# Kernel tuning notes

Measured on AMD Instinct MI355X. Metric: run time of the kernel, lower is better.

Reference implementation:

```python
import jax, jax.numpy as jnp
import numpy as np

LN_EPS = 1e-5


def _gather(x, idx):
    # x: [B, N, C], idx: [B, N, K] -> [B, N, K, C]
    return jax.vmap(lambda xb, ib: xb[ib])(x, idx)


def setup_inputs() -> dict:
    key = jax.random.key(0)
    ks = jax.random.split(key, 8)
    B, N, K, C_in, C_out, GEO = 2, 16384, 32, 128, 128, 10
    return {
        "points": jax.random.normal(ks[0], (B, N, 3), dtype=jnp.float32),
        "features": jax.random.normal(ks[1], (B, N, C_in), dtype=jnp.float32),
        "grouped_idx": jax.random.randint(ks[2], (B, N, K), 0, N, dtype=jnp.int32),
        "w_pos": jax.random.normal(ks[3], (GEO, C_in), dtype=jnp.float32) * (GEO ** -0.5),
        "b_pos": jnp.zeros((C_in,), jnp.float32),
        "w_gcm": jax.random.normal(ks[4], (C_in, C_in), dtype=jnp.float32) * (C_in ** -0.5),
        "b_gcm": jnp.zeros((C_in,), jnp.float32),
        "w_out": jax.random.normal(ks[5], (C_in, C_out), dtype=jnp.float32) * (C_in ** -0.5),
        "b_out": jnp.zeros((C_out,), jnp.float32),
        "ln_g": jnp.ones((C_out,), jnp.float32),
        "ln_b": jnp.zeros((C_out,), jnp.float32),
    }


def reference(points, features, grouped_idx, w_pos, b_pos, w_gcm, b_gcm,
              w_out, b_out, ln_g, ln_b):
    # gather neighbor coords and features: [B, N, K, *]
    grouped_pts = _gather(points, grouped_idx)
    xyz = points[..., 0:3]                      # [B, N, 3]
    grouped_xyz = grouped_pts[..., 0:3]         # [B, N, K, 3]
    center = xyz[:, :, None, :]                 # [B, N, 1, 3]
    diff = grouped_xyz - center                 # xi - xj
    dist = jnp.linalg.norm(diff, axis=-1, keepdims=True)  # ||xi - xj||
    K = grouped_xyz.shape[2]
    geo = jnp.concatenate(
        [jnp.broadcast_to(center, grouped_xyz.shape), grouped_xyz, diff, dist],
        axis=-1)                                # [B, N, K, 10]
    expanded_f = geo @ w_pos + b_pos            # pos_proj -> [B, N, K, C_in]
    grouped_f = _gather(features, grouped_idx)  # [B, N, K, C_in]
    h = jax.nn.relu((grouped_f + expanded_f) @ w_gcm + b_gcm)  # gcm_layer
    pooled = jnp.max(h, axis=2)                 # maxpooling over neighbors
    res = pooled + features                     # residual
    o = res @ w_out + b_out                     # out Linear
    mu = jnp.mean(o, axis=-1, keepdims=True)
    var = jnp.mean((o - mu) ** 2, axis=-1, keepdims=True)
    o = (o - mu) * jax.lax.rsqrt(var + LN_EPS) * ln_g + ln_b  # LayerNorm
    return jax.nn.relu(o)
```

## Files before the change

### kernel.cpp

```cpp
#include <hip/hip_runtime.h>
#include <hip/hip_bf16.h>
#include <math.h>

typedef __attribute__((ext_vector_type(8))) short short8;
typedef __attribute__((ext_vector_type(4))) short short4v;
typedef __attribute__((ext_vector_type(4))) float float4v;
typedef unsigned short ushort_t;

constexpr int NPTS = 32768;
constexpr int NN   = 16384;
constexpr int KK   = 32;
constexpr int CC   = 128;
constexpr int GRP  = 16;
constexpr int SG2  = 24;
constexpr int SR   = 136;
#define LN_EPS 1e-5f
#define MFMA   __builtin_amdgcn_mfma_f32_16x16x32_bf16

constexpr size_t WS_WP   = 0;
constexpr size_t WS_WO   = 40960;
constexpr size_t WS_BE   = 73728;
constexpr size_t WS_PG   = 74240;
constexpr size_t WS_FB   = 79360;
constexpr size_t WS_NEED = WS_FB + (size_t)NPTS * CC * 2;

__device__ __forceinline__ short f2bs(float x) {
    return (short)__builtin_bit_cast(unsigned short, __float2bfloat16(x));
}
__device__ __forceinline__ float bs2f(ushort_t u) {
    return __uint_as_float(((unsigned)u) << 16);
}

__global__ __launch_bounds__(128) void prep_fold(
    const float* __restrict__ w_pos, const float* __restrict__ b_pos,
    const float* __restrict__ w_gcm, const float* __restrict__ b_gcm,
    float* __restrict__ wsPG, float* __restrict__ wsBeff)
{
    const int c = threadIdx.x, g = blockIdx.x;
    if (g < 10) {
        float s = 0.f;
        #pragma unroll
        for (int r = 0; r < 128; ++r) s += w_pos[g * 128 + r] * w_gcm[r * 128 + c];
        wsPG[g * 128 + c] = s;
    } else {
        float s = b_gcm[c];
        #pragma unroll
        for (int r = 0; r < 128; ++r) s += b_pos[r] * w_gcm[r * 128 + c];
        wsBeff[c] = s;
    }
}

__global__ __launch_bounds__(256) void prep_pack(
    const float* __restrict__ features, const float* __restrict__ w_gcm,
    const float* __restrict__ w_out, const float* __restrict__ wsPG,
    short* __restrict__ wsWp, short* __restrict__ wsWo, ushort_t* __restrict__ featbf,
    int do_convert)
{
    const int t = threadIdx.x, blk = blockIdx.x;
    if (blk < 512) {
        if (!do_convert) return;
        const int base = blk * 2048 + t;
        #pragma unroll
        for (int i = 0; i < 8; ++i) {
            const int f4 = base + i * 256;
            const float4 a = ((const float4*)features)[f4];
            short4v v; v[0]=f2bs(a.x); v[1]=f2bs(a.y); v[2]=f2bs(a.z); v[3]=f2bs(a.w);
            ((short4v*)featbf)[f4] = v;
        }
        return;
    }
    if (blk == 512) {
        #pragma unroll 4
        for (int e = t; e < 16 * 128 * 8; e += 256) {
            const int j = e & 7, n = (e >> 3) & 127, g = e >> 10;
            wsWp[e] = f2bs(w_gcm[(g * 8 + j) * 128 + n]);
        }
        return;
    }
    if (blk == 513) {
        #pragma unroll 4
        for (int e2 = t; e2 < 4 * 128 * 8; e2 += 256) {
            const int e = 16 * 128 * 8 + e2;
            const int j = e & 7, n = (e >> 3) & 127, g = e >> 10;
            const int k = g * 8 + j;
            wsWp[e] = (k < 138) ? f2bs(wsPG[(k - 128) * 128 + n]) : (short)0;
        }
        return;
    }
    #pragma unroll 4
    for (int e = t; e < 128 * 128; e += 256) {
        const int j = e & 7, n = (e >> 3) & 127, g = e >> 10;
        wsWo[e] = f2bs(w_out[(g * 8 + j) * 128 + n]);
    }
}

template<int FB>
__global__ __launch_bounds__(256, 3) void bridge_main(
    const float* __restrict__ points, const float* __restrict__ features,
    const int*   __restrict__ gidx,
    const short* __restrict__ wsWp, const short* __restrict__ wsWo,
    const float* __restrict__ wsBeff, const ushort_t* __restrict__ featbf,
    const float* __restrict__ b_out, const float* __restrict__ ln_g,
    const float* __restrict__ ln_b,
    float* __restrict__ out)
{
    __shared__ short sA[4][KK * CC];
    __shared__ short sG[3][KK * SG2];
    __shared__ short sRes[GRP * SR];
    __shared__ short sResF[GRP * CC];
    __shared__ int   sIdx[GRP * KK];
    __shared__ float sCtr[GRP * 3];
    __shared__ float sPS[4][GRP], sPQ[4][GRP];

    const int t = threadIdx.x, wv = t >> 6, lane = t & 63;
    const int quad = (lane >> 4) & 3, m = lane & 15;
    const int g0 = blockIdx.x * GRP;
    const int nbase = (g0 >= NN) ? NN : 0;
    const int col0 = wv * 32 + m;

    sIdx[t]       = gidx[(size_t)g0 * KK + t];
    sIdx[t + 256] = gidx[(size_t)g0 * KK + t + 256];
    if (t < GRP * 3) sCtr[t] = points[(size_t)g0 * 3 + t];
    if constexpr (FB) {
        const ushort_t* rs = featbf + (size_t)g0 * CC + (wv * 64 + lane) * 8;
        short* rd = sResF + wv * 512;
        __builtin_amdgcn_global_load_lds((const __attribute__((address_space(1))) void*)rs,
                                         (__attribute__((address_space(3))) void*)rd, 16, 0, 0);
    } else {
        const float* fs = features + (size_t)g0 * CC + t * 8;
        short8 v;
        #pragma unroll
        for (int i = 0; i < 8; ++i) v[i] = f2bs(fs[i]);
        *(short8*)&sResF[t * 8] = v;
    }

    short8 bWp[5][2];
    #pragma unroll
    for (int ks = 0; ks < 5; ++ks)
        #pragma unroll
        for (int ntl = 0; ntl < 2; ++ntl)
            bWp[ks][ntl] = *((const short8*)wsWp + ((ks * 4 + quad) * 128 + col0 + ntl * 16));
    const float beffv[2] = { wsBeff[col0], wsBeff[col0 + 16] };

    __syncthreads();

    const int r0 = wv * 4 + (lane >> 4);
    const int pc = lane & 15;
    const int gc = pc ^ r0;

    float geoS[3][3];

    auto geo_load = [&](int q) {
        if (lane < 8) {
            const int j = wv * 8 + lane;
            const int kng = nbase + sIdx[q * KK + j];
            const float* pp = points + (size_t)kng * 3;
            const int s = q % 3;
            geoS[s][0] = pp[0]; geoS[s][1] = pp[1]; geoS[s][2] = pp[2];
        }
    };
    auto issue_dma = [&](int q) {
        const int buf = q & 3;
        const int kn0 = nbase + sIdx[q * KK + r0];
        const int kn1 = nbase + sIdx[q * KK + r0 + 16];
        if constexpr (FB) {
            const ushort_t* gp0 = featbf + (size_t)kn0 * CC + gc * 8;
            const ushort_t* gp1 = featbf + (size_t)kn1 * CC + gc * 8;
            short* l0 = &sA[buf][(wv * 4) * CC];
            short* l1 = &sA[buf][(wv * 4 + 16) * CC];
            __builtin_amdgcn_global_load_lds((const __attribute__((address_space(1))) void*)gp0,
                                             (__attribute__((address_space(3))) void*)l0, 16, 0, 0);
            __builtin_amdgcn_global_load_lds((const __attribute__((address_space(1))) void*)gp1,
                                             (__attribute__((address_space(3))) void*)l1, 16, 0, 0);
        } else {
            const float4* f0 = (const float4*)(features + (size_t)kn0 * CC + gc * 8);
            const float4* f1 = (const float4*)(features + (size_t)kn1 * CC + gc * 8);
            const float4 a = f0[0], b = f0[1], c = f1[0], d = f1[1];
            short8 v;
            v[0]=f2bs(a.x); v[1]=f2bs(a.y); v[2]=f2bs(a.z); v[3]=f2bs(a.w);
            v[4]=f2bs(b.x); v[5]=f2bs(b.y); v[6]=f2bs(b.z); v[7]=f2bs(b.w);
            *(short8*)&sA[buf][r0 * CC + pc * 8] = v;
            v[0]=f2bs(c.x); v[1]=f2bs(c.y); v[2]=f2bs(c.z); v[3]=f2bs(c.w);
            v[4]=f2bs(d.x); v[5]=f2bs(d.y); v[6]=f2bs(d.z); v[7]=f2bs(d.w);
            *(short8*)&sA[buf][(r0 + 16) * CC + pc * 8] = v;
        }
    };
    auto geo_store = [&](int q) {
        if (lane < 8) {
            const int j = wv * 8 + lane, s = q % 3, b = q % 3;
            const float cx = sCtr[q * 3], cy = sCtr[q * 3 + 1], cz = sCtr[q * 3 + 2];
            const float gx = geoS[s][0], gy = geoS[s][1], gz = geoS[s][2];
            const float dx = gx - cx, dy = gy - cy, dz = gz - cz;
            const float dist = sqrtf(dx * dx + dy * dy + dz * dz);
            short8 v0, v1 = (short8)0;
            v0[0]=f2bs(cx); v0[1]=f2bs(cy); v0[2]=f2bs(cz);
            v0[3]=f2bs(gx); v0[4]=f2bs(gy); v0[5]=f2bs(gz);
            v0[6]=f2bs(dx); v0[7]=f2bs(dy);
            v1[0]=f2bs(dz); v1[1]=f2bs(dist);
            *(short8*)&sG[b][j * SG2 + 0] = v0;
            *(short8*)&sG[b][j * SG2 + 8] = v1;
        }
    };

    int offA[4];
    #pragma unroll
    for (int ks = 0; ks < 4; ++ks) offA[ks] = m * CC + (((ks * 4 + quad) ^ m) * 8);
    const int offG = m * SG2 + quad * 8;

    auto compute = [&](int p) {
        const short* ab = sA[p & 3];
        const short* ag = sG[p % 3];
        float4v acc[2][2] = {};
        #pragma unroll
        for (int ks = 0; ks < 4; ++ks) {
            const short8 a0 = *(const short8*)(ab + offA[ks]);
            const short8 a1 = *(const short8*)(ab + offA[ks] + 16 * CC);
            acc[0][0] = MFMA(a0, bWp[ks][0], acc[0][0], 0, 0, 0);
            acc[0][1] = MFMA(a0, bWp[ks][1], acc[0][1], 0, 0, 0);
            acc[1][0] = MFMA(a1, bWp[ks][0], acc[1][0], 0, 0, 0);
            acc[1][1] = MFMA(a1, bWp[ks][1], acc[1][1], 0, 0, 0);
        }
        short8 ga0 = (short8)0, ga1 = (short8)0;
        if (quad < 2) {
            ga0 = *(const short8*)(ag + offG);
            ga1 = *(const short8*)(ag + offG + 16 * SG2);
        }
        acc[0][0] = MFMA(ga0, bWp[4][0], acc[0][0], 0, 0, 0);
        acc[0][1] = MFMA(ga0, bWp[4][1], acc[0][1], 0, 0, 0);
        acc[1][0] = MFMA(ga1, bWp[4][0], acc[1][0], 0, 0, 0);
        acc[1][1] = MFMA(ga1, bWp[4][1], acc[1][1], 0, 0, 0);

        #pragma unroll
        for (int ntl = 0; ntl < 2; ++ntl) {
            float v = acc[0][ntl][0];
            #pragma unroll
            for (int rr = 1; rr < 4; ++rr) v = fmaxf(v, acc[0][ntl][rr]);
            #pragma unroll
            for (int rr = 0; rr < 4; ++rr) v = fmaxf(v, acc[1][ntl][rr]);
            v = fmaxf(v, __shfl_xor(v, 16));
            v = fmaxf(v, __shfl_xor(v, 32));
            v = fmaxf(v + beffv[ntl], 0.f);
            if (quad == 0) {
                const float fc = bs2f((ushort_t)sResF[p * CC + col0 + ntl * 16]);
                sRes[p * SR + col0 + ntl * 16] = f2bs(v + fc);
            }
        }
    };

    geo_load(0); issue_dma(0);
    geo_load(1); issue_dma(1);
    geo_load(2); issue_dma(2);
    geo_store(0);
    geo_store(1);
    __syncthreads();

    #pragma unroll
    for (int p = 0; p < GRP; ++p) {
        if (p > 0) {
            if (p == GRP - 1) asm volatile("s_waitcnt vmcnt(0)" ::: "memory");
            asm volatile("s_waitcnt lgkmcnt(0)" ::: "memory");
            __builtin_amdgcn_s_barrier();
        }
        __builtin_amdgcn_sched_barrier(0);
        if (p + 3 < GRP) { geo_load(p + 3); issue_dma(p + 3); }
        compute(p);
        if (p + 2 < GRP) geo_store(p + 2);
    }

    __syncthreads();

    short8 bWo[4][2];
    #pragma unroll
    for (int ks = 0; ks < 4; ++ks)
        #pragma unroll
        for (int ntl = 0; ntl < 2; ++ntl)
            bWo[ks][ntl] = *((const short8*)wsWo + ((ks * 4 + quad) * 128 + col0 + ntl * 16));

    const short* rm = sRes + m * SR;
    float4v acc2[2] = {};
    #pragma unroll
    for (int ks = 0; ks < 4; ++ks) {
        const short8 a = *(const short8*)(rm + ks * 32 + quad * 8);
        acc2[0] = MFMA(a, bWo[ks][0], acc2[0], 0, 0, 0);
        acc2[1] = MFMA(a, bWo[ks][1], acc2[1], 0, 0, 0);
    }

    const float boutv[2] = { b_out[col0], b_out[col0 + 16] };
    const float lngv[2]  = { ln_g[col0], ln_g[col0 + 16] };
    const float lnbv[2]  = { ln_b[col0], ln_b[col0 + 16] };

    #pragma unroll
    for (int r = 0; r < 4; ++r) {
        const float o0 = acc2[0][r] + boutv[0];
        const float o1 = acc2[1][r] + boutv[1];
        float ss = o0 + o1, qq = o0 * o0 + o1 * o1;
        #pragma unroll
        for (int d = 1; d < 16; d <<= 1) { ss += __shfl_xor(ss, d); qq += __shfl_xor(qq, d); }
        if (m == 0) { sPS[wv][quad * 4 + r] = ss; sPQ[wv][quad * 4 + r] = qq; }
    }
    __syncthreads();

    #pragma unroll
    for (int r = 0; r < 4; ++r) {
        const int R = quad * 4 + r;
        const float S = sPS[0][R] + sPS[1][R] + sPS[2][R] + sPS[3][R];
        const float Q = sPQ[0][R] + sPQ[1][R] + sPQ[2][R] + sPQ[3][R];
        const float mu  = S * (1.f / 128.f);
        const float var = fmaxf(Q * (1.f / 128.f) - mu * mu, 0.f);
        const float rstd = rsqrtf(var + LN_EPS);
        const float o0 = acc2[0][r] + boutv[0];
        const float o1 = acc2[1][r] + boutv[1];
        const size_t base = (size_t)(g0 + R) * CC;
        out[base + col0]      = fmaxf((o0 - mu) * rstd * lngv[0] + lnbv[0], 0.f);
        out[base + col0 + 16] = fmaxf((o1 - mu) * rstd * lngv[1] + lnbv[1], 0.f);
    }
}

extern "C" void kernel_launch(void* const* d_in, const int* in_sizes, int n_in,
                              void* d_out, int out_size, void* d_ws, size_t ws_size,
                              hipStream_t stream) {
    const float* points   = (const float*)d_in[0];
    const float* features = (const float*)d_in[1];
    const int*   gidx     = (const int*)  d_in[2];
    const float* w_pos    = (const float*)d_in[3];
    const float* b_pos    = (const float*)d_in[4];
    const float* w_gcm    = (const float*)d_in[5];
    const float* b_gcm    = (const float*)d_in[6];
    const float* w_out    = (const float*)d_in[7];
    const float* b_out    = (const float*)d_in[8];
    const float* ln_g     = (const float*)d_in[9];
    const float* ln_b     = (const float*)d_in[10];
    float* out = (float*)d_out;

    char* ws = (char*)d_ws;
    short*    wsWp   = (short*)(ws + WS_WP);
    short*    wsWo   = (short*)(ws + WS_WO);
    float*    wsBeff = (float*)(ws + WS_BE);
    float*    wsPG   = (float*)(ws + WS_PG);
    ushort_t* featbf = (ushort_t*)(ws + WS_FB);

    const bool use_bf = (ws_size >= WS_NEED);

    hipLaunchKernelGGL(prep_fold, dim3(11), dim3(128), 0, stream,
                       w_pos, b_pos, w_gcm, b_gcm, wsPG, wsBeff);
    hipLaunchKernelGGL(prep_pack, dim3(515), dim3(256), 0, stream,
                       features, w_gcm, w_out, wsPG, wsWp, wsWo, featbf,
                       use_bf ? 1 : 0);
    if (use_bf) {
        hipLaunchKernelGGL((bridge_main<1>), dim3(NPTS / GRP), dim3(256), 0, stream,
                           points, features, gidx, wsWp, wsWo, wsBeff, featbf,
                           b_out, ln_g, ln_b, out);
    } else {
        hipLaunchKernelGGL((bridge_main<0>), dim3(NPTS / GRP), dim3(256), 0, stream,
                           points, features, gidx, wsWp, wsWo, wsBeff, featbf,
                           b_out, ln_g, ln_b, out);
    }
}
```

Baseline: 163.3 us.

## Precompute per-point features times W_gcm and gather projected rows instead

Uses linearity to compute F·W_gcm once per point in a prep kernel (N×C×C work instead of N×K×C×C), so the main kernel gathers the already-projected bf16 rows and only adds a small rank-4 geometric MFMA plus a per-center correction before the max-pool. The geometry weights are folded so that center, neighbor and diff terms collapse into neighbor xyz, dist and a per-center bias. Gathered rows are read with transposed LDS loads directly into MFMA accumulator layout. This moves the large GEMM out of the per-neighbor loop, at the cost of an extra prep pass over features and a bf16 rounding of the projected values.

Measured after the change: 169.2 us. 3.6% more time.

```diff
diff --git a/kernel.cpp b/kernel.cpp
--- a/kernel.cpp
+++ b/kernel.cpp
@@ -5,6 +5,7 @@
 typedef __attribute__((ext_vector_type(8))) short short8;
 typedef __attribute__((ext_vector_type(4))) short short4v;
 typedef __attribute__((ext_vector_type(4))) float float4v;
+typedef __attribute__((ext_vector_type(2))) unsigned int uint2v;
 typedef unsigned short ushort_t;
 
 constexpr int NPTS = 32768;
@@ -12,17 +13,22 @@
 constexpr int KK   = 32;
 constexpr int CC   = 128;
 constexpr int GRP  = 16;
+constexpr int SR   = 136;
 constexpr int SG2  = 24;
-constexpr int SR   = 136;
 #define LN_EPS 1e-5f
 #define MFMA   __builtin_amdgcn_mfma_f32_16x16x32_bf16
-
-constexpr size_t WS_WP   = 0;
-constexpr size_t WS_WO   = 40960;
-constexpr size_t WS_BE   = 73728;
-constexpr size_t WS_PG   = 74240;
-constexpr size_t WS_FB   = 79360;
-constexpr size_t WS_NEED = WS_FB + (size_t)NPTS * CC * 2;
+#define GLL(src, dst, sz) __builtin_amdgcn_global_load_lds( \
+    (const __attribute__((address_space(1))) void*)(src),   \
+    (__attribute__((address_space(3))) void*)(dst), sz, 0, 0)
+
+constexpr size_t WS_FW  = 0;
+constexpr size_t WS_WO  = (size_t)NPTS * CC * 2;
+constexpr size_t WS_BE  = WS_WO + 32768;
+constexpr size_t WS_W4  = WS_BE + 512;
+constexpr size_t WS_WC  = WS_W4 + 2048;
+constexpr size_t WS_WPF = WS_WC + 1536;
+constexpr size_t WS_NEED = WS_WPF + 32768;
+constexpr size_t FB_WP = 0, FB_WO = 40960, FB_BE = 73728, FB_PG = 74240;
 
 __device__ __forceinline__ short f2bs(float x) {
     return (short)__builtin_bit_cast(unsigned short, __float2bfloat16(x));
@@ -31,7 +37,283 @@
     return __uint_as_float(((unsigned)u) << 16);
 }
 
-__global__ __launch_bounds__(128) void prep_fold(
+__global__ __launch_bounds__(256) void prep_w(
+    const float* __restrict__ w_gcm, const float* __restrict__ w_out,
+    const float* __restrict__ w_pos, const float* __restrict__ b_pos,
+    const float* __restrict__ b_gcm,
+    short* __restrict__ wsWpF, short* __restrict__ wsWo,
+    float* __restrict__ wsBeff, short* __restrict__ wsW4, float* __restrict__ wsWc)
+{
+    const int t = threadIdx.x, blk = blockIdx.x;
+    __shared__ float sPG[10 * 128];
+    if (blk == 0) {
+        #pragma unroll 4
+        for (int e = t; e < 16 * 128 * 8; e += 256) {
+            const int j = e & 7, n = (e >> 3) & 127, g = e >> 10;
+            wsWpF[e] = f2bs(w_gcm[(g * 8 + j) * 128 + n]);
+        }
+    } else if (blk == 1) {
+        #pragma unroll 4
+        for (int e = t; e < 128 * 128; e += 256) {
+            const int j = e & 7, n = (e >> 3) & 127, g = e >> 10;
+            wsWo[e] = f2bs(w_out[(g * 8 + j) * 128 + n]);
+        }
+    } else {
+        if (t < 128) {
+            const int c = t;
+            for (int g = 0; g < 10; ++g) {
+                float s = 0.f;
+                for (int r = 0; r < 128; ++r) s += w_pos[g * 128 + r] * w_gcm[r * 128 + c];
+                sPG[g * 128 + c] = s;
+            }
+            float sb = b_gcm[c];
+            for (int r = 0; r < 128; ++r) sb += b_pos[r] * w_gcm[r * 128 + c];
+            wsBeff[c] = sb;
+        }
+        __syncthreads();
+        if (t < 128) {
+            const int c = t;
+            short8 v = (short8)0;
+            v[0] = f2bs(sPG[3 * 128 + c] + sPG[6 * 128 + c]);
+            v[1] = f2bs(sPG[4 * 128 + c] + sPG[7 * 128 + c]);
+            v[2] = f2bs(sPG[5 * 128 + c] + sPG[8 * 128 + c]);
+            v[3] = f2bs(sPG[9 * 128 + c]);
+            *(short8*)&wsW4[c * 8] = v;
+            wsWc[0 * 128 + c] = sPG[0 * 128 + c] - sPG[6 * 128 + c];
+            wsWc[1 * 128 + c] = sPG[1 * 128 + c] - sPG[7 * 128 + c];
+            wsWc[2 * 128 + c] = sPG[2 * 128 + c] - sPG[8 * 128 + c];
+        }
+    }
+}
+
+__global__ __launch_bounds__(256) void prep_fw(
+    const float* __restrict__ features, const short* __restrict__ wsWpF,
+    ushort_t* __restrict__ wsFW)
+{
+    const int t = threadIdx.x, blk = blockIdx.x;
+    __shared__ short sF[16 * SR];
+    const int g0 = blk * GRP;
+    {
+        const int row = t >> 4, c8 = (t & 15) * 8;
+        const float* fp = features + (size_t)(g0 + row) * CC + c8;
+        const float4 a = *(const float4*)fp;
+        const float4 b = *(const float4*)(fp + 4);
+        short8 v;
+        v[0]=f2bs(a.x); v[1]=f2bs(a.y); v[2]=f2bs(a.z); v[3]=f2bs(a.w);
+        v[4]=f2bs(b.x); v[5]=f2bs(b.y); v[6]=f2bs(b.z); v[7]=f2bs(b.w);
+        *(short8*)&sF[row * SR + c8] = v;
+    }
+    const int wv = t >> 6, lane = t & 63, quad = (lane >> 4) & 3, m = lane & 15;
+    const int col0 = wv * 32 + m;
+    short8 bf[4][2];
+    #pragma unroll
+    for (int ks = 0; ks < 4; ++ks) {
+        bf[ks][0] = *((const short8*)wsWpF + ((ks * 4 + quad) * 128 + col0));
+        bf[ks][1] = *((const short8*)wsWpF + ((ks * 4 + quad) * 128 + col0 + 16));
+    }
+    __syncthreads();
+    float4v acc[2] = {};
+    #pragma unroll
+    for (int ks = 0; ks < 4; ++ks) {
+        const short8 a = *(const short8*)(sF + m * SR + ks * 32 + quad * 8);
+        acc[0] = MFMA(a, bf[ks][0], acc[0], 0, 0, 0);
+        acc[1] = MFMA(a, bf[ks][1], acc[1], 0, 0, 0);
+    }
+    #pragma unroll
+    for (int r = 0; r < 4; ++r) {
+        const int R = quad * 4 + r;
+        wsFW[(size_t)(g0 + R) * CC + col0]      = (ushort_t)f2bs(acc[0][r]);
+        wsFW[(size_t)(g0 + R) * CC + col0 + 16] = (ushort_t)f2bs(acc[1][r]);
+    }
+}
+
+__global__ __launch_bounds__(256, 3) void bridge_fw(
+    const float* __restrict__ points, const float* __restrict__ features,
+    const int*   __restrict__ gidx,
+    const short* __restrict__ wsWo, const float* __restrict__ wsBeff,
+    const short* __restrict__ wsW4, const float* __restrict__ wsWc,
+    const ushort_t* __restrict__ wsFW,
+    const float* __restrict__ b_out, const float* __restrict__ ln_g,
+    const float* __restrict__ ln_b, float* __restrict__ out)
+{
+    __shared__ short sA[4][3][1024];
+    __shared__ float sGxyz[GRP * KK * 3];
+    __shared__ short sRes[GRP * SR];
+    __shared__ short sResF[GRP * CC];
+    __shared__ int   sIdx[GRP * KK];
+    __shared__ float sCtr[GRP * 3];
+    __shared__ float sPS[4][GRP], sPQ[4][GRP];
+
+    const int t = threadIdx.x, wv = t >> 6, lane = t & 63;
+    const int q = (lane >> 4) & 3, m = lane & 15;
+    const int g0 = blockIdx.x * GRP;
+    const int nbase = (g0 >= NN) ? NN : 0;
+    const int colA = wv * 32 + m;
+    const int rbL = lane >> 3, jL = (lane & 7) >> 1, hL = lane & 1;
+
+    {
+        const int gA = gidx[(size_t)g0 * KK + t];
+        const int gB = gidx[(size_t)g0 * KK + t + 256];
+        sIdx[t] = gA; sIdx[t + 256] = gB;
+        const float* pA = points + (size_t)(nbase + gA) * 3;
+        const float* pB = points + (size_t)(nbase + gB) * 3;
+        sGxyz[t * 3 + 0] = pA[0]; sGxyz[t * 3 + 1] = pA[1]; sGxyz[t * 3 + 2] = pA[2];
+        sGxyz[(t + 256) * 3 + 0] = pB[0];
+        sGxyz[(t + 256) * 3 + 1] = pB[1];
+        sGxyz[(t + 256) * 3 + 2] = pB[2];
+    }
+    if (t < GRP * 3) sCtr[t] = points[(size_t)g0 * 3 + t];
+    {
+        const int row = t >> 4, c8 = (t & 15) * 8;
+        const float* fp = features + (size_t)(g0 + row) * CC + c8;
+        const float4 a = *(const float4*)fp;
+        const float4 b = *(const float4*)(fp + 4);
+        short8 v;
+        v[0]=f2bs(a.x); v[1]=f2bs(a.y); v[2]=f2bs(a.z); v[3]=f2bs(a.w);
+        v[4]=f2bs(b.x); v[5]=f2bs(b.y); v[6]=f2bs(b.z); v[7]=f2bs(b.w);
+        *(short8*)&sResF[row * CC + c8] = v;
+    }
+
+    const float beffv[2] = { wsBeff[colA], wsBeff[colA + 16] };
+    float wc[6];
+    #pragma unroll
+    for (int i = 0; i < 3; ++i) { wc[i] = wsWc[i * 128 + colA]; wc[3 + i] = wsWc[i * 128 + colA + 16]; }
+    short8 w4f[2];
+    #pragma unroll
+    for (int n = 0; n < 2; ++n) {
+        const short8 w = *((const short8*)wsW4 + (colA + n * 16));
+        w4f[n] = (q == 0) ? w : (short8)0;
+    }
+    const unsigned trBase = (unsigned)(size_t)(__attribute__((address_space(3))) short*)&sA[wv][0][0]
+                          + (unsigned)(lane * 8);
+
+    __syncthreads();
+
+    auto issue_fw = [&](int p, int buf) {
+        const int kw = nbase + sIdx[p * KK + rbL * 4 + jL];
+        const ushort_t* s0 = wsFW + (size_t)kw * CC + wv * 32 + hL * 8;
+        GLL(s0,      &sA[wv][buf][0],   16);
+        GLL(s0 + 16, &sA[wv][buf][512], 16);
+    };
+
+    issue_fw(0, 0);
+    issue_fw(1, 1);
+
+    #pragma unroll
+    for (int p = 0; p < GRP; ++p) {
+        const int buf = p % 3;
+        if (p + 2 < GRP) issue_fw(p + 2, (p + 2) % 3);
+        if (p + 2 < GRP)      asm volatile("s_waitcnt vmcnt(4)" ::: "memory");
+        else if (p + 1 < GRP) asm volatile("s_waitcnt vmcnt(2)" ::: "memory");
+        else                  asm volatile("s_waitcnt vmcnt(0)" ::: "memory");
+        __builtin_amdgcn_sched_barrier(0);
+
+        uint2v t00, t10, t01, t11;
+        const unsigned trA = trBase + (unsigned)(buf * 2048);
+        asm volatile("ds_read_b64_tr_b16 %0, %1 offset:0"    : "=&v"(t00) : "v"(trA));
+        asm volatile("ds_read_b64_tr_b16 %0, %1 offset:512"  : "=&v"(t10) : "v"(trA));
+        asm volatile("ds_read_b64_tr_b16 %0, %1 offset:1024" : "=&v"(t01) : "v"(trA));
+        asm volatile("ds_read_b64_tr_b16 %0, %1 offset:1536" : "=&v"(t11) : "v"(trA));
+
+        const float pcx = sCtr[p * 3], pcy = sCtr[p * 3 + 1], pcz = sCtr[p * 3 + 2];
+        short8 ga0 = (short8)0, ga1 = (short8)0;
+        if (q == 0) {
+            const int i0 = (p * KK + m) * 3, i1 = i0 + 48;
+            const float ax = sGxyz[i0], ay = sGxyz[i0 + 1], az = sGxyz[i0 + 2];
+            const float bx = sGxyz[i1], by = sGxyz[i1 + 1], bz = sGxyz[i1 + 2];
+            const float d0x = ax - pcx, d0y = ay - pcy, d0z = az - pcz;
+            const float d1x = bx - pcx, d1y = by - pcy, d1z = bz - pcz;
+            const float s0 = sqrtf(d0x * d0x + d0y * d0y + d0z * d0z);
+            const float s1 = sqrtf(d1x * d1x + d1y * d1y + d1z * d1z);
+            ga0[0]=f2bs(ax); ga0[1]=f2bs(ay); ga0[2]=f2bs(az); ga0[3]=f2bs(s0);
+            ga1[0]=f2bs(bx); ga1[1]=f2bs(by); ga1[2]=f2bs(bz); ga1[3]=f2bs(s1);
+        }
+
+        asm volatile("s_waitcnt lgkmcnt(0)" ::: "memory");
+        __builtin_amdgcn_sched_barrier(0);
+
+        float4v c00, c10, c01, c11;
+        c00[0]=__uint_as_float(t00[0] << 16); c00[1]=__uint_as_float(t00[0] & 0xffff0000u);
+        c00[2]=__uint_as_float(t00[1] << 16); c00[3]=__uint_as_float(t00[1] & 0xffff0000u);
+        c10[0]=__uint_as_float(t10[0] << 16); c10[1]=__uint_as_float(t10[0] & 0xffff0000u);
+        c10[2]=__uint_as_float(t10[1] << 16); c10[3]=__uint_as_float(t10[1] & 0xffff0000u);
+        c01[0]=__uint_as_float(t01[0] << 16); c01[1]=__uint_as_float(t01[0] & 0xffff0000u);
+        c01[2]=__uint_as_float(t01[1] << 16); c01[3]=__uint_as_float(t01[1] & 0xffff0000u);
+        c11[0]=__uint_as_float(t11[0] << 16); c11[1]=__uint_as_float(t11[0] & 0xffff0000u);
+        c11[2]=__uint_as_float(t11[1] << 16); c11[3]=__uint_as_float(t11[1] & 0xffff0000u);
+
+        c00 = MFMA(ga0, w4f[0], c00, 0, 0, 0);
+        c01 = MFMA(ga0, w4f[1], c01, 0, 0, 0);
+        c10 = MFMA(ga1, w4f[0], c10, 0, 0, 0);
+        c11 = MFMA(ga1, w4f[1], c11, 0, 0, 0);
+
+        const float cb0 = pcx * wc[0] + pcy * wc[1] + pcz * wc[2];
+        const float cb1 = pcx * wc[3] + pcy * wc[4] + pcz * wc[5];
+
+        float v0 = fmaxf(fmaxf(fmaxf(c00[0],c00[1]), fmaxf(c00[2],c00[3])),
+                         fmaxf(fmaxf(c10[0],c10[1]), fmaxf(c10[2],c10[3])));
+        float v1 = fmaxf(fmaxf(fmaxf(c01[0],c01[1]), fmaxf(c01[2],c01[3])),
+                         fmaxf(fmaxf(c11[0],c11[1]), fmaxf(c11[2],c11[3])));
+        v0 = fmaxf(v0, __shfl_xor(v0, 16)); v0 = fmaxf(v0, __shfl_xor(v0, 32));
+        v1 = fmaxf(v1, __shfl_xor(v1, 16)); v1 = fmaxf(v1, __shfl_xor(v1, 32));
+        v0 = fmaxf(v0 + beffv[0] + cb0, 0.f);
+        v1 = fmaxf(v1 + beffv[1] + cb1, 0.f);
+        if (q == 0) {
+            sRes[p * SR + colA]      = f2bs(v0 + bs2f((ushort_t)sResF[p * CC + colA]));
+            sRes[p * SR + colA + 16] = f2bs(v1 + bs2f((ushort_t)sResF[p * CC + colA + 16]));
+        }
+    }
+
+    __syncthreads();
+
+    short8 bWo[4][2];
+    #pragma unroll
+    for (int ks = 0; ks < 4; ++ks)
+        #pragma unroll
+        for (int ntl = 0; ntl < 2; ++ntl)
+            bWo[ks][ntl] = *((const short8*)wsWo + ((ks * 4 + q) * 128 + colA + ntl * 16));
+
+    const short* rm = sRes + m * SR;
+    float4v acc2[2] = {};
+    #pragma unroll
+    for (int ks = 0; ks < 4; ++ks) {
+        const short8 a = *(const short8*)(rm + ks * 32 + q * 8);
+        acc2[0] = MFMA(a, bWo[ks][0], acc2[0], 0, 0, 0);
+        acc2[1] = MFMA(a, bWo[ks][1], acc2[1], 0, 0, 0);
+    }
+
+    const float boutv[2] = { b_out[colA], b_out[colA + 16] };
+    const float lngv[2]  = { ln_g[colA], ln_g[colA + 16] };
+    const float lnbv[2]  = { ln_b[colA], ln_b[colA + 16] };
+
+    #pragma unroll
+    for (int r = 0; r < 4; ++r) {
+        const float o0 = acc2[0][r] + boutv[0];
+        const float o1 = acc2[1][r] + boutv[1];
+        float ss = o0 + o1, qq = o0 * o0 + o1 * o1;
+        #pragma unroll
+        for (int d = 1; d < 16; d <<= 1) { ss += __shfl_xor(ss, d); qq += __shfl_xor(qq, d); }
+        if (m == 0) { sPS[wv][q * 4 + r] = ss; sPQ[wv][q * 4 + r] = qq; }
+    }
+    __syncthreads();
+
+    #pragma unroll
+    for (int r = 0; r < 4; ++r) {
+        const int R = q * 4 + r;
+        const float S = sPS[0][R] + sPS[1][R] + sPS[2][R] + sPS[3][R];
+        const float Q = sPQ[0][R] + sPQ[1][R] + sPQ[2][R] + sPQ[3][R];
+        const float mu  = S * (1.f / 128.f);
+        const float var = fmaxf(Q * (1.f / 128.f) - mu * mu, 0.f);
+        const float rstd = rsqrtf(var + LN_EPS);
+        const float o0 = acc2[0][r] + boutv[0];
+        const float o1 = acc2[1][r] + boutv[1];
+        const size_t base = (size_t)(g0 + R) * CC;
+        out[base + colA]      = fmaxf((o0 - mu) * rstd * lngv[0] + lnbv[0], 0.f);
+        out[base + colA + 16] = fmaxf((o1 - mu) * rstd * lngv[1] + lnbv[1], 0.f);
+    }
+}
+
+__global__ __launch_bounds__(128) void prep_fold_fb(
     const float* __restrict__ w_pos, const float* __restrict__ b_pos,
     const float* __restrict__ w_gcm, const float* __restrict__ b_gcm,
     float* __restrict__ wsPG, float* __restrict__ wsBeff)
@@ -39,45 +321,27 @@
     const int c = threadIdx.x, g = blockIdx.x;
     if (g < 10) {
         float s = 0.f;
-        #pragma unroll
         for (int r = 0; r < 128; ++r) s += w_pos[g * 128 + r] * w_gcm[r * 128 + c];
         wsPG[g * 128 + c] = s;
     } else {
         float s = b_gcm[c];
-        #pragma unroll
         for (int r = 0; r < 128; ++r) s += b_pos[r] * w_gcm[r * 128 + c];
         wsBeff[c] = s;
     }
 }
 
-__global__ __launch_bounds__(256) void prep_pack(
-    const float* __restrict__ features, const float* __restrict__ w_gcm,
-    const float* __restrict__ w_out, const float* __restrict__ wsPG,
-    short* __restrict__ wsWp, short* __restrict__ wsWo, ushort_t* __restrict__ featbf,
-    int do_convert)
+__global__ __launch_bounds__(256) void prep_pack_fb(
+    const float* __restrict__ w_gcm, const float* __restrict__ w_out,
+    const float* __restrict__ wsPG, short* __restrict__ wsWp, short* __restrict__ wsWo)
 {
     const int t = threadIdx.x, blk = blockIdx.x;
-    if (blk < 512) {
-        if (!do_convert) return;
-        const int base = blk * 2048 + t;
-        #pragma unroll
-        for (int i = 0; i < 8; ++i) {
-            const int f4 = base + i * 256;
-            const float4 a = ((const float4*)features)[f4];
-            short4v v; v[0]=f2bs(a.x); v[1]=f2bs(a.y); v[2]=f2bs(a.z); v[3]=f2bs(a.w);
-            ((short4v*)featbf)[f4] = v;
-        }
-        return;
-    }
-    if (blk == 512) {
+    if (blk == 0) {
         #pragma unroll 4
         for (int e = t; e < 16 * 128 * 8; e += 256) {
             const int j = e & 7, n = (e >> 3) & 127, g = e >> 10;
             wsWp[e] = f2bs(w_gcm[(g * 8 + j) * 128 + n]);
         }
-        return;
-    }
-    if (blk == 513) {
+    } else if (blk == 1) {
         #pragma unroll 4
         for (int e2 = t; e2 < 4 * 128 * 8; e2 += 256) {
             const int e = 16 * 128 * 8 + e2;
@@ -85,24 +349,22 @@
             const int k = g * 8 + j;
             wsWp[e] = (k < 138) ? f2bs(wsPG[(k - 128) * 128 + n]) : (short)0;
         }
-        return;
-    }
-    #pragma unroll 4
-    for (int e = t; e < 128 * 128; e += 256) {
-        const int j = e & 7, n = (e >> 3) & 127, g = e >> 10;
-        wsWo[e] = f2bs(w_out[(g * 8 + j) * 128 + n]);
-    }
-}
-
-template<int FB>
-__global__ __launch_bounds__(256, 3) void bridge_main(
+    } else {
+        #pragma unroll 4
+        for (int e = t; e < 128 * 128; e += 256) {
+            const int j = e & 7, n = (e >> 3) & 127, g = e >> 10;
+            wsWo[e] = f2bs(w_out[(g * 8 + j) * 128 + n]);
+        }
+    }
+}
+
+__global__ __launch_bounds__(256, 3) void bridge_fb(
     const float* __restrict__ points, const float* __restrict__ features,
     const int*   __restrict__ gidx,
     const short* __restrict__ wsWp, const short* __restrict__ wsWo,
-    const float* __restrict__ wsBeff, const ushort_t* __restrict__ featbf,
+    const float* __restrict__ wsBeff,
     const float* __restrict__ b_out, const float* __restrict__ ln_g,
-    const float* __restrict__ ln_b,
-    float* __restrict__ out)
+    const float* __restrict__ ln_b, float* __restrict__ out)
 {
     __shared__ short sA[4][KK * CC];
     __shared__ short sG[3][KK * SG2];
@@ -121,12 +383,7 @@
     sIdx[t]       = gidx[(size_t)g0 * KK + t];
     sIdx[t + 256] = gidx[(size_t)g0 * KK + t + 256];
     if (t < GRP * 3) sCtr[t] = points[(size_t)g0 * 3 + t];
-    if constexpr (FB) {
-        const ushort_t* rs = featbf + (size_t)g0 * CC + (wv * 64 + lane) * 8;
-        short* rd = sResF + wv * 512;
-        __builtin_amdgcn_global_load_lds((const __attribute__((address_space(1))) void*)rs,
-                                         (__attribute__((address_space(3))) void*)rd, 16, 0, 0);
-    } else {
+    {
         const float* fs = features + (size_t)g0 * CC + t * 8;
         short8 v;
         #pragma unroll
@@ -150,45 +407,34 @@
 
     float geoS[3][3];
 
-    auto geo_load = [&](int q) {
+    auto geo_load = [&](int qq) {
         if (lane < 8) {
             const int j = wv * 8 + lane;
-            const int kng = nbase + sIdx[q * KK + j];
+            const int kng = nbase + sIdx[qq * KK + j];
             const float* pp = points + (size_t)kng * 3;
-            const int s = q % 3;
+            const int s = qq % 3;
             geoS[s][0] = pp[0]; geoS[s][1] = pp[1]; geoS[s][2] = pp[2];
         }
     };
-    auto issue_dma = [&](int q) {
-        const int buf = q & 3;
-        const int kn0 = nbase + sIdx[q * KK + r0];
-        const int kn1 = nbase + sIdx[q * KK + r0 + 16];
-        if constexpr (FB) {
-            const ushort_t* gp0 = featbf + (size_t)kn0 * CC + gc * 8;
-            const ushort_t* gp1 = featbf + (size_t)kn1 * CC + gc * 8;
-            short* l0 = &sA[buf][(wv * 4) * CC];
-            short* l1 = &sA[buf][(wv * 4 + 16) * CC];
-            __builtin_amdgcn_global_load_lds((const __attribute__((address_space(1))) void*)gp0,
-                                             (__attribute__((address_space(3))) void*)l0, 16, 0, 0);
-            __builtin_amdgcn_global_load_lds((const __attribute__((address_space(1))) void*)gp1,
-                                             (__attribute__((address_space(3))) void*)l1, 16, 0, 0);
-        } else {
-            const float4* f0 = (const float4*)(features + (size_t)kn0 * CC + gc * 8);
-            const float4* f1 = (const float4*)(features + (size_t)kn1 * CC + gc * 8);
-            const float4 a = f0[0], b = f0[1], c = f1[0], d = f1[1];
-            short8 v;
-            v[0]=f2bs(a.x); v[1]=f2bs(a.y); v[2]=f2bs(a.z); v[3]=f2bs(a.w);
-            v[4]=f2bs(b.x); v[5]=f2bs(b.y); v[6]=f2bs(b.z); v[7]=f2bs(b.w);
-            *(short8*)&sA[buf][r0 * CC + pc * 8] = v;
-            v[0]=f2bs(c.x); v[1]=f2bs(c.y); v[2]=f2bs(c.z); v[3]=f2bs(c.w);
-            v[4]=f2bs(d.x); v[5]=f2bs(d.y); v[6]=f2bs(d.z); v[7]=f2bs(d.w);
-            *(short8*)&sA[buf][(r0 + 16) * CC + pc * 8] = v;
-        }
+    auto stage = [&](int qq) {
+        const int buf = qq & 3;
+        const int kn0 = nbase + sIdx[qq * KK + r0];
+        const int kn1 = nbase + sIdx[qq * KK + r0 + 16];
+        const float4* f0 = (const float4*)(features + (size_t)kn0 * CC + gc * 8);
+        const float4* f1 = (const float4*)(features + (size_t)kn1 * CC + gc * 8);
+        const float4 a = f0[0], b = f0[1], c = f1[0], d = f1[1];
+        short8 v;
+        v[0]=f2bs(a.x); v[1]=f2bs(a.y); v[2]=f2bs(a.z); v[3]=f2bs(a.w);
+        v[4]=f2bs(b.x); v[5]=f2bs(b.y); v[6]=f2bs(b.z); v[7]=f2bs(b.w);
+        *(short8*)&sA[buf][r0 * CC + pc * 8] = v;
+        v[0]=f2bs(c.x); v[1]=f2bs(c.y); v[2]=f2bs(c.z); v[3]=f2bs(c.w);
+        v[4]=f2bs(d.x); v[5]=f2bs(d.y); v[6]=f2bs(d.z); v[7]=f2bs(d.w);
+        *(short8*)&sA[buf][(r0 + 16) * CC + pc * 8] = v;
     };
-    auto geo_store = [&](int q) {
+    auto geo_store = [&](int qq) {
         if (lane < 8) {
-            const int j = wv * 8 + lane, s = q % 3, b = q % 3;
-            const float cx = sCtr[q * 3], cy = sCtr[q * 3 + 1], cz = sCtr[q * 3 + 2];
+            const int j = wv * 8 + lane, s = qq % 3, b = qq % 3;
+            const float cx = sCtr[qq * 3], cy = sCtr[qq * 3 + 1], cz = sCtr[qq * 3 + 2];
             const float gx = geoS[s][0], gy = geoS[s][1], gz = geoS[s][2];
             const float dx = gx - cx, dy = gy - cy, dz = gz - cz;
             const float dist = sqrtf(dx * dx + dy * dy + dz * dz);
@@ -207,7 +453,21 @@
     for (int ks = 0; ks < 4; ++ks) offA[ks] = m * CC + (((ks * 4 + quad) ^ m) * 8);
     const int offG = m * SG2 + quad * 8;
 
-    auto compute = [&](int p) {
+    geo_load(0); stage(0);
+    geo_load(1); stage(1);
+    geo_load(2); stage(2);
+    geo_store(0); geo_store(1);
+    __syncthreads();
+
+    #pragma unroll
+    for (int p = 0; p < GRP; ++p) {
+        if (p > 0) {
+            asm volatile("s_waitcnt lgkmcnt(0)" ::: "memory");
+            __builtin_amdgcn_s_barrier();
+        }
+        __builtin_amdgcn_sched_barrier(0);
+        if (p + 3 < GRP) { geo_load(p + 3); stage(p + 3); }
+
         const short* ab = sA[p & 3];
         const short* ag = sG[p % 3];
         float4v acc[2][2] = {};
@@ -245,25 +505,6 @@
                 sRes[p * SR + col0 + ntl * 16] = f2bs(v + fc);
             }
         }
-    };
-
-    geo_load(0); issue_dma(0);
-    geo_load(1); issue_dma(1);
-    geo_load(2); issue_dma(2);
-    geo_store(0);
-    geo_store(1);
-    __syncthreads();
-
-    #pragma unroll
-    for (int p = 0; p < GRP; ++p) {
-        if (p > 0) {
-            if (p == GRP - 1) asm volatile("s_waitcnt vmcnt(0)" ::: "memory");
-            asm volatile("s_waitcnt lgkmcnt(0)" ::: "memory");
-            __builtin_amdgcn_s_barrier();
-        }
-        __builtin_amdgcn_sched_barrier(0);
-        if (p + 3 < GRP) { geo_load(p + 3); issue_dma(p + 3); }
-        compute(p);
         if (p + 2 < GRP) geo_store(p + 2);
     }
 
@@ -284,22 +525,19 @@
         acc2[0] = MFMA(a, bWo[ks][0], acc2[0], 0, 0, 0);
         acc2[1] = MFMA(a, bWo[ks][1], acc2[1], 0, 0, 0);
     }
-
     const float boutv[2] = { b_out[col0], b_out[col0 + 16] };
     const float lngv[2]  = { ln_g[col0], ln_g[col0 + 16] };
     const float lnbv[2]  = { ln_b[col0], ln_b[col0 + 16] };
-
     #pragma unroll
     for (int r = 0; r < 4; ++r) {
         const float o0 = acc2[0][r] + boutv[0];
         const float o1 = acc2[1][r] + boutv[1];
-        float ss = o0 + o1, qq = o0 * o0 + o1 * o1;
-        #pragma unroll
-        for (int d = 1; d < 16; d <<= 1) { ss += __shfl_xor(ss, d); qq += __shfl_xor(qq, d); }
-        if (m == 0) { sPS[wv][quad * 4 + r] = ss; sPQ[wv][quad * 4 + r] = qq; }
-    }
-    __syncthreads();
-
+        float ss = o0 + o1, qq2 = o0 * o0 + o1 * o1;
+        #pragma unroll
+        for (int d = 1; d < 16; d <<= 1) { ss += __shfl_xor(ss, d); qq2 += __shfl_xor(qq2, d); }
+        if (m == 0) { sPS[wv][quad * 4 + r] = ss; sPQ[wv][quad * 4 + r] = qq2; }
+    }
+    __syncthreads();
     #pragma unroll
     for (int r = 0; r < 4; ++r) {
         const int R = quad * 4 + r;
@@ -331,28 +569,34 @@
     const float* ln_g     = (const float*)d_in[9];
     const float* ln_b     = (const float*)d_in[10];
     float* out = (float*)d_out;
-
     char* ws = (char*)d_ws;
-    short*    wsWp   = (short*)(ws + WS_WP);
-    short*    wsWo   = (short*)(ws + WS_WO);
-    float*    wsBeff = (float*)(ws + WS_BE);
-    float*    wsPG   = (float*)(ws + WS_PG);
-    ushort_t* featbf = (ushort_t*)(ws + WS_FB);
-
-    const bool use_bf = (ws_size >= WS_NEED);
-
-    hipLaunchKernelGGL(prep_fold, dim3(11), dim3(128), 0, stream,
-                       w_pos, b_pos, w_gcm, b_gcm, wsPG, wsBeff);
-    hipLaunchKernelGGL(prep_pack, dim3(515), dim3(256), 0, stream,
-                       features, w_gcm, w_out, wsPG, wsWp, wsWo, featbf,
-                       use_bf ? 1 : 0);
-    if (use_bf) {
-        hipLaunchKernelGGL((bridge_main<1>), dim3(NPTS / GRP), dim3(256), 0, stream,
-                           points, features, gidx, wsWp, wsWo, wsBeff, featbf,
+
+    if (ws_size >= WS_NEED) {
+        ushort_t* wsFW   = (ushort_t*)(ws + WS_FW);
+        short*    wsWo   = (short*)(ws + WS_WO);
+        float*    wsBeff = (float*)(ws + WS_BE);
+        short*    wsW4   = (short*)(ws + WS_W4);
+        float*    wsWc   = (float*)(ws + WS_WC);
+        short*    wsWpF  = (short*)(ws + WS_WPF);
+        hipLaunchKernelGGL(prep_w, dim3(3), dim3(256), 0, stream,
+                           w_gcm, w_out, w_pos, b_pos, b_gcm,
+                           wsWpF, wsWo, wsBeff, wsW4, wsWc);
+        hipLaunchKernelGGL(prep_fw, dim3(NPTS / GRP), dim3(256), 0, stream,
+                           features, wsWpF, wsFW);
+        hipLaunchKernelGGL(bridge_fw, dim3(NPTS / GRP), dim3(256), 0, stream,
+                           points, features, gidx, wsWo, wsBeff, wsW4, wsWc, wsFW,
                            b_out, ln_g, ln_b, out);
     } else {
-        hipLaunchKernelGGL((bridge_main<0>), dim3(NPTS / GRP), dim3(256), 0, stream,
-                           points, features, gidx, wsWp, wsWo, wsBeff, featbf,
+        short* wsWp   = (short*)(ws + FB_WP);
+        short* wsWo   = (short*)(ws + FB_WO);
+        float* wsBeff = (float*)(ws + FB_BE);
+        float* wsPG   = (float*)(ws + FB_PG);
+        hipLaunchKernelGGL(prep_fold_fb, dim3(11), dim3(128), 0, stream,
+                           w_pos, b_pos, w_gcm, b_gcm, wsPG, wsBeff);
+        hipLaunchKernelGGL(prep_pack_fb, dim3(3), dim3(256), 0, stream,
+                           w_gcm, w_out, wsPG, wsWp, wsWo);
+        hipLaunchKernelGGL(bridge_fb, dim3(NPTS / GRP), dim3(256), 0, stream,
+                           points, features, gidx, wsWp, wsWo, wsBeff,
                            b_out, ln_g, ln_b, out);
     }
 }
```
